# Performance work log

Hardware: AMD Instinct MI355X
Metric: run time of the kernel (lower is better)

## Reference

```python
import jax, jax.numpy as jnp
import numpy as np

B, T, F1, F2 = 16384, 5, 300, 251
IN, H = 551, 128

def setup_inputs() -> dict:
    key = jax.random.key(0)
    ks = jax.random.split(key, 16)
    s = 0.05
    return {
        "x1": jax.random.normal(ks[0], (B, T, F1), jnp.float32),
        "x2": jax.random.normal(ks[1], (B, T, F2), jnp.float32),
        "W_ih": jax.random.normal(ks[2], (4 * H, IN), jnp.float32) * s,
        "W_hh": jax.random.normal(ks[3], (4 * H, H), jnp.float32) * s,
        "b_ih": jax.random.normal(ks[4], (4 * H,), jnp.float32) * s,
        "b_hh": jax.random.normal(ks[5], (4 * H,), jnp.float32) * s,
        "W1": jax.random.normal(ks[6], (531, H * T), jnp.float32) * s,
        "b1": jax.random.normal(ks[7], (531,), jnp.float32) * s,
        "W2": jax.random.normal(ks[8], (256, 531), jnp.float32) * s,
        "b2": jax.random.normal(ks[9], (256,), jnp.float32) * s,
        "W3": jax.random.normal(ks[10], (64, 256), jnp.float32) * s,
        "b3": jax.random.normal(ks[11], (64,), jnp.float32) * s,
        "W4": jax.random.normal(ks[12], (2, 64), jnp.float32) * s,
        "b4": jax.random.normal(ks[13], (2,), jnp.float32) * s,
    }

def _lstm(x, W_ih, W_hh, b_ih, b_hh):
    # x: [B, T, IN] -> outputs [B, T, H]; PyTorch gate order i, f, g, o
    xg = jnp.einsum('bti,gi->btg', x, W_ih) + b_ih + b_hh  # [B, T, 4H]
    xg = jnp.transpose(xg, (1, 0, 2))  # [T, B, 4H]
    h0 = jnp.zeros((x.shape[0], H), x.dtype)
    c0 = jnp.zeros((x.shape[0], H), x.dtype)

    def step(carry, xg_t):
        h, c = carry
        g = xg_t + h @ W_hh.T  # [B, 4H]
        i, f, gg, o = jnp.split(g, 4, axis=-1)
        c = jax.nn.sigmoid(f) * c + jax.nn.sigmoid(i) * jnp.tanh(gg)
        h = jax.nn.sigmoid(o) * jnp.tanh(c)
        return (h, c), h

    _, hs = jax.lax.scan(step, (h0, c0), xg)  # hs: [T, B, H]
    return jnp.transpose(hs, (1, 0, 2))

def reference(x1, x2, W_ih, W_hh, b_ih, b_hh, W1, b1, W2, b2, W3, b3, W4, b4):
    x = jnp.concatenate((x1, x2), axis=2)  # [B, T, 551]
    h = _lstm(x, W_ih, W_hh, b_ih, b_hh)   # [B, T, H]
    h = h.reshape(h.shape[0], T * H)
    h = jax.nn.relu(h @ W1.T + b1)
    h = jax.nn.relu(h @ W2.T + b2)
    h = jax.nn.relu(h @ W3.T + b3)
    logits = h @ W4.T + b4
    return jax.nn.softmax(logits, axis=1)
```

## Files before the change

kernel.cpp:

```cpp
#include <hip/hip_runtime.h>
#include <hip/hip_bf16.h>


typedef short  short8  __attribute__((ext_vector_type(8)));
typedef short  short4v __attribute__((ext_vector_type(4)));
typedef float  f32x4   __attribute__((ext_vector_type(4)));

#define MFMA(a, b, c) __builtin_amdgcn_mfma_f32_16x16x32_bf16((a), (b), (c), 0, 0, 0)
#define WAITV(N) asm volatile("s_waitcnt vmcnt(" #N ")" ::: "memory")
#define LGKM0()  asm volatile("s_waitcnt lgkmcnt(0)" ::: "memory")
#define MEMF()   asm volatile("" ::: "memory")
#define BAR()    __builtin_amdgcn_s_barrier()

__device__ __forceinline__ short f2bs(float f) {
    __hip_bfloat16 h = __float2bfloat16(f);
    union { __hip_bfloat16 h; short s; } u; u.h = h; return u.s;
}
__device__ __forceinline__ float b2f(short s) {
    union { unsigned u; float f; } v; v.u = ((unsigned)(unsigned short)s) << 16; return v.f;
}
__device__ __forceinline__ float sigf(float x)  { return 1.f / (1.f + __expf(-x)); }
__device__ __forceinline__ float mytanh(float x){ return 2.f / (1.f + __expf(-2.f * x)) - 1.f; }

__device__ __forceinline__ void gload16(const void* g, void* l) {
    __builtin_amdgcn_global_load_lds(
        (const __attribute__((address_space(1))) void*)g,
        (__attribute__((address_space(3))) void*)l, 16, 0, 0);
}

#define BB     16384
#define TT     5
#define F1     300
#define F2     251
#define INF    551
#define KP     576
#define G4     512
#define HH     128
#define FLAT   640
#define L1N    531
#define L1P    576
#define L1KP   544
#define L2N    256
#define L3N    64

#define O_WIH  0u
#define O_WHH  589824u
#define O_W1   720896u
#define O_W2   1458176u
#define O_W3   1736704u
#define O_BG   1769472u
#define O_B1   1771520u
#define O_XG   1773824u
#define O_HS   85659904u
#define WS_NEED 106631424u

__device__ __forceinline__ void pack_b(const float* __restrict__ W, short* __restrict__ dst,
                                       int i, int tpn, int Nsrc, int Ksrc, int ldw)
{
    int tile = i >> 9, rem = i & 511, lane = rem >> 3, jj = rem & 7;
    int tn = tile / tpn, tk = tile - tn * tpn;
    int n = tn * 16 + (lane & 15);
    int k = tk * 32 + (lane >> 4) * 8 + jj;
    float v = (n < Nsrc && k < Ksrc) ? W[n * ldw + k] : 0.f;
    dst[i] = f2bs(v);
}

__device__ __forceinline__ void pack_bih(const float* __restrict__ W, short* __restrict__ dst,
                                         int i)
{
    int tile = i >> 9, rem = i & 511, lane = rem >> 3, jj = rem & 7;
    int tn = tile / 18, tk = tile - tn * 18;
    int n = tn * 16 + (lane & 15);
    int k = tk * 32 + (lane >> 4) * 8 + jj;
    int keff = (k <= 546) ? k : (k >= 548 && k <= 551) ? (k - 1) : -1;
    float v = (keff >= 0) ? W[n * INF + keff] : 0.f;
    dst[i] = f2bs(v);
}

__global__ void prep_kernel(
    const float* __restrict__ W_ih, const float* __restrict__ W_hh,
    const float* __restrict__ b_ih, const float* __restrict__ b_hh,
    const float* __restrict__ W1,   const float* __restrict__ b1,
    const float* __restrict__ W2,   const float* __restrict__ W3,
    short* __restrict__ Wihp, short* __restrict__ Whhp, float* __restrict__ biasg,
    short* __restrict__ W1p,  float* __restrict__ b1p,  short* __restrict__ W2p,
    short* __restrict__ W3p)
{
    const int N0 = G4 * KP;
    const int N1 = N0 + G4 * HH;
    const int N2 = N1 + L1P * FLAT;
    const int N3 = N2 + L2N * L1KP;
    const int N4 = N3 + L3N * L2N;
    const int N5 = N4 + G4;
    const int N6 = N5 + L1P;
    const int stride = gridDim.x * blockDim.x;
    for (int i = blockIdx.x * blockDim.x + threadIdx.x; i < N6; i += stride) {
        if (i < N0)      pack_bih(W_ih, Wihp, i);
        else if (i < N1) pack_b(W_hh, Whhp, i - N0,   4, G4,  HH,  HH);
        else if (i < N2) pack_b(W1,   W1p,  i - N1,  20, L1N, FLAT, FLAT);
        else if (i < N3) pack_b(W2,   W2p,  i - N2,  17, L2N, L1N, L1N);
        else if (i < N4) pack_b(W3,   W3p,  i - N3,   8, L3N, L2N, L2N);
        else if (i < N5) { int j = i - N4; biasg[j] = b_ih[j] + b_hh[j]; }
        else             { int j = i - N5; b1p[j] = (j < L1N) ? b1[j] : 0.f; }
    }
}

__device__ __forceinline__ float4 ld4r(const float* __restrict__ x1r,
                                       const float* __restrict__ x2r, int c)
{
    const float* p = (c < F1) ? (x1r + c) : (x2r + (c - F1));
    return *(const float4*)p;
}

__global__ __launch_bounds__(256, 3) void k1_xgemm(
    const float* __restrict__ x1, const float* __restrict__ x2,
    const short* __restrict__ Wihp, const float* __restrict__ biasg,
    short* __restrict__ xg)
{
    __shared__ __align__(16) short As[128][32];
    __shared__ __align__(16) short Bs[8][512];
    const int tid  = threadIdx.x;
    const int w    = tid >> 6;
    const int lane = tid & 63;
    const int c16  = lane & 15;
    const int kq   = lane >> 4;
    const int wm   = w >> 1, wn = w & 1;

    const int id  = blockIdx.x;
    const int mp  = (id & 7) * 80 + ((id >> 3) >> 2);
    const int nb  = (id >> 3) & 3;
    const int m0  = mp * 128;
    const int t   = m0 >> 14;
    const int bb  = m0 & 16383;

    const int sr = tid >> 1, sh = tid & 1;
    const int arow = bb + sr;
    const float* x1r = x1 + ((size_t)arow * TT + t) * F1;
    const float* x2r = x2 + ((size_t)arow * TT + t) * F2;
    const int fA = (sr >> 1) & 3;
    short* d0 = &As[sr][(((sh << 1)    ) ^ fA) << 3];
    short* d1 = &As[sr][(((sh << 1) | 1) ^ fA) << 3];

    f32x4 acc[4][4];
#pragma unroll
    for (int mt = 0; mt < 4; ++mt)
#pragma unroll
        for (int nt = 0; nt < 4; ++nt)
            acc[mt][nt] = (f32x4){0.f, 0.f, 0.f, 0.f};

    for (int s = 0; s < 18; ++s) {
        BAR(); MEMF();
#pragma unroll
        for (int i2 = 0; i2 < 2; ++i2) {
            int tnl = w * 2 + i2;
            gload16(Wihp + (((nb * 8 + tnl) * 18 + s) << 9) + lane * 8,
                    &Bs[tnl][0]);
        }
        float4 q0, q1, q2, q3;
        if (s < 17) {
            int c0 = s * 32 + sh * 16;
            q0 = ld4r(x1r, x2r, c0);
            q1 = ld4r(x1r, x2r, c0 + 4);
            q2 = ld4r(x1r, x2r, c0 + 8);
            q3 = ld4r(x1r, x2r, c0 + 12);
        } else {
            if (sh == 0) {
                q0 = *(const float4*)(x2r + 244);
                q1 = *(const float4*)(x2r + 247);
            } else {
                q0 = (float4){0.f, 0.f, 0.f, 0.f};
                q1 = q0;
            }
            q2 = (float4){0.f, 0.f, 0.f, 0.f};
            q3 = q2;
        }
        {
            short8 v0, v1;
            v0[0] = f2bs(q0.x); v0[1] = f2bs(q0.y); v0[2] = f2bs(q0.z); v0[3] = f2bs(q0.w);
            v0[4] = f2bs(q1.x); v0[5] = f2bs(q1.y); v0[6] = f2bs(q1.z); v0[7] = f2bs(q1.w);
            v1[0] = f2bs(q2.x); v1[1] = f2bs(q2.y); v1[2] = f2bs(q2.z); v1[3] = f2bs(q2.w);
            v1[4] = f2bs(q3.x); v1[5] = f2bs(q3.y); v1[6] = f2bs(q3.z); v1[7] = f2bs(q3.w);
            *(short8*)d0 = v0;
            *(short8*)d1 = v1;
        }
        WAITV(0); LGKM0(); BAR(); MEMF();

        short8 a[4];
#pragma unroll
        for (int mt = 0; mt < 4; ++mt) {
            int r = (wm * 4 + mt) * 16 + c16;
            a[mt] = *(const short8*)&As[r][(kq ^ ((r >> 1) & 3)) << 3];
        }
#pragma unroll
        for (int nt = 0; nt < 4; ++nt) {
            short8 b = *(const short8*)&Bs[wn * 4 + nt][lane * 8];
#pragma unroll
            for (int mt = 0; mt < 4; ++mt)
                acc[mt][nt] = MFMA(a[mt], b, acc[mt][nt]);
        }
    }

#pragma unroll
    for (int nt = 0; nt < 4; ++nt) {
        int tn = nb * 8 + wn * 4 + nt;
        float bv = biasg[tn * 16 + c16];
#pragma unroll
        for (int mt = 0; mt < 4; ++mt) {
            short4v o;
#pragma unroll
            for (int r = 0; r < 4; ++r) o[r] = f2bs(acc[mt][nt][r] + bv);
            int tm = (m0 >> 4) + wm * 4 + mt;
            *(short4v*)&xg[((tm * 32 + tn) << 8) + lane * 4] = o;
        }
    }
}

__global__ __launch_bounds__(512, 2) void k2_rec(
    const short* __restrict__ Whhp, const short* __restrict__ xg,
    short* __restrict__ hs)
{
    __shared__ __align__(16) short hb[2][32][136];
    const int tid  = threadIdx.x;
    const int w    = tid >> 6;
    const int lane = tid & 63;
    const int quad = lane >> 4;
    const int c16  = lane & 15;
    const int btile = blockIdx.x * 2;

    short8 bfr[4][4];
#pragma unroll
    for (int g = 0; g < 4; ++g)
#pragma unroll
        for (int ks = 0; ks < 4; ++ks)
            bfr[g][ks] = *(const short8*)&Whhp[((((g * 8 + w) * 4) + ks) << 9) + lane * 8];

    float cst[2][4];
#pragma unroll
    for (int mt = 0; mt < 2; ++mt)
#pragma unroll
        for (int r = 0; r < 4; ++r) cst[mt][r] = 0.f;

    const int j = w * 16 + c16;

    for (int t = 0; t < TT; ++t) {
        short4v xq[2][4];
#pragma unroll
        for (int mt = 0; mt < 2; ++mt)
#pragma unroll
            for (int g = 0; g < 4; ++g)
                xq[mt][g] = *(const short4v*)
                    &xg[((((t << 10) + btile + mt) * 32 + (g * 8 + w)) << 8) + lane * 4];

        f32x4 acc[2][4];
#pragma unroll
        for (int mt = 0; mt < 2; ++mt)
#pragma unroll
            for (int g = 0; g < 4; ++g)
                acc[mt][g] = (f32x4){0.f, 0.f, 0.f, 0.f};

        if (t > 0) {
            const short (*cur)[136] = hb[(t - 1) & 1];
#pragma unroll
            for (int ks = 0; ks < 4; ++ks) {
                short8 a[2];
#pragma unroll
                for (int mt = 0; mt < 2; ++mt)
                    a[mt] = *(const short8*)&cur[mt * 16 + c16][ks * 32 + quad * 8];
#pragma unroll
                for (int mt = 0; mt < 2; ++mt)
#pragma unroll
                    for (int g = 0; g < 4; ++g)
                        acc[mt][g] = MFMA(a[mt], bfr[g][ks], acc[mt][g]);
            }
        }

        short (*nxt)[136] = hb[t & 1];
#pragma unroll
        for (int mt = 0; mt < 2; ++mt) {
#pragma unroll
            for (int r = 0; r < 4; ++r) {
                int m = mt * 16 + quad * 4 + r;
                float gi = acc[mt][0][r] + b2f(xq[mt][0][r]);
                float gf = acc[mt][1][r] + b2f(xq[mt][1][r]);
                float gg = acc[mt][2][r] + b2f(xq[mt][2][r]);
                float go = acc[mt][3][r] + b2f(xq[mt][3][r]);
                float cn = sigf(gf) * cst[mt][r] + sigf(gi) * mytanh(gg);
                cst[mt][r] = cn;
                nxt[m][j] = f2bs(sigf(go) * mytanh(cn));
            }
        }
        __syncthreads();
        {
            int tm = w >> 2, kt = w & 3;
            short8 v = *(const short8*)&nxt[tm * 16 + c16][kt * 32 + quad * 8];
            *(short8*)&hs[(((btile + tm) * 20 + t * 4 + kt) << 9) + lane * 8] = v;
        }
    }
}

__global__ __launch_bounds__(256, 2) void mlp_kernel(
    const short* __restrict__ hs,
    const short* __restrict__ W1p, const float* __restrict__ b1p,
    const short* __restrict__ W2p, const float* __restrict__ b2,
    const short* __restrict__ W3p, const float* __restrict__ b3,
    const float* __restrict__ W4,  const float* __restrict__ b4,
    float* __restrict__ out)
{
    __shared__ __align__(16) short a1[32][584];
    __shared__ __align__(16) short a2[32][264];
    __shared__ __align__(16) short a3[32][72];
    const int tid  = threadIdx.x;
    const int w    = tid >> 6;
    const int lane = tid & 63;
    const int quad = lane >> 4;
    const int c16  = lane & 15;
    const int m0   = blockIdx.x * 32;
    const int mtile = blockIdx.x * 2;

    {
        f32x4 acc[2][9];
#pragma unroll
        for (int mt = 0; mt < 2; ++mt)
#pragma unroll
            for (int i = 0; i < 9; ++i)
                acc[mt][i] = (f32x4){0.f, 0.f, 0.f, 0.f};
#pragma unroll 4
        for (int ks = 0; ks < 20; ++ks) {
            short8 a[2];
#pragma unroll
            for (int mt = 0; mt < 2; ++mt)
                a[mt] = *(const short8*)&hs[(((mtile + mt) * 20 + ks) << 9) + lane * 8];
#pragma unroll
            for (int i = 0; i < 9; ++i) {
                short8 b = *(const short8*)&W1p[(((w * 9 + i) * 20 + ks) << 9) + lane * 8];
                acc[0][i] = MFMA(a[0], b, acc[0][i]);
                acc[1][i] = MFMA(a[1], b, acc[1][i]);
            }
        }
#pragma unroll
        for (int i = 0; i < 9; ++i) {
            int n = (w * 9 + i) * 16 + c16;
            float bv = b1p[n];
#pragma unroll
            for (int mt = 0; mt < 2; ++mt)
#pragma unroll
                for (int r = 0; r < 4; ++r) {
                    int m = mt * 16 + quad * 4 + r;
                    float v = acc[mt][i][r] + bv;
                    a1[m][n] = f2bs(v > 0.f ? v : 0.f);
                }
        }
    }
    __syncthreads();

    {
        f32x4 acc[2][4];
#pragma unroll
        for (int mt = 0; mt < 2; ++mt)
#pragma unroll
            for (int i = 0; i < 4; ++i)
                acc[mt][i] = (f32x4){0.f, 0.f, 0.f, 0.f};
#pragma unroll 4
        for (int ks = 0; ks < 17; ++ks) {
            short8 a[2];
#pragma unroll
            for (int mt = 0; mt < 2; ++mt)
                a[mt] = *(const short8*)&a1[mt * 16 + c16][ks * 32 + quad * 8];
#pragma unroll
            for (int i = 0; i < 4; ++i) {
                short8 b = *(const short8*)&W2p[(((w * 4 + i) * 17 + ks) << 9) + lane * 8];
                acc[0][i] = MFMA(a[0], b, acc[0][i]);
                acc[1][i] = MFMA(a[1], b, acc[1][i]);
            }
        }
#pragma unroll
        for (int i = 0; i < 4; ++i) {
            int n = (w * 4 + i) * 16 + c16;
            float bv = b2[n];
#pragma unroll
            for (int mt = 0; mt < 2; ++mt)
#pragma unroll
                for (int r = 0; r < 4; ++r) {
                    int m = mt * 16 + quad * 4 + r;
                    float v = acc[mt][i][r] + bv;
                    a2[m][n] = f2bs(v > 0.f ? v : 0.f);
                }
        }
    }
    __syncthreads();

    {
        f32x4 acc[2];
        acc[0] = (f32x4){0.f, 0.f, 0.f, 0.f};
        acc[1] = (f32x4){0.f, 0.f, 0.f, 0.f};
#pragma unroll
        for (int ks = 0; ks < 8; ++ks) {
            short8 a[2];
#pragma unroll
            for (int mt = 0; mt < 2; ++mt)
                a[mt] = *(const short8*)&a2[mt * 16 + c16][ks * 32 + quad * 8];
            short8 b = *(const short8*)&W3p[((w * 8 + ks) << 9) + lane * 8];
            acc[0] = MFMA(a[0], b, acc[0]);
            acc[1] = MFMA(a[1], b, acc[1]);
        }
        int n = w * 16 + c16;
        float bv = b3[n];
#pragma unroll
        for (int mt = 0; mt < 2; ++mt)
#pragma unroll
            for (int r = 0; r < 4; ++r) {
                int m = mt * 16 + quad * 4 + r;
                float v = acc[mt][r] + bv;
                a3[m][n] = f2bs(v > 0.f ? v : 0.f);
            }
    }
    __syncthreads();

    if (tid < 64) {
        int m   = tid >> 1;
        int cls = tid & 1;
        float s = b4[cls];
#pragma unroll 8
        for (int k = 0; k < 64; ++k)
            s += b2f(a3[m][k]) * W4[cls * 64 + k];
        float other = __shfl_xor(s, 1);
        float p = 1.f / (1.f + __expf(other - s));
        out[(m0 + m) * 2 + cls] = p;
    }
}

extern "C" void kernel_launch(void* const* d_in, const int* in_sizes, int n_in,
                              void* d_out, int out_size, void* d_ws, size_t ws_size,
                              hipStream_t stream)
{
    (void)in_sizes; (void)n_in; (void)out_size;
    if (ws_size < (size_t)WS_NEED) return;

    const float* x1   = (const float*)d_in[0];
    const float* x2   = (const float*)d_in[1];
    const float* W_ih = (const float*)d_in[2];
    const float* W_hh = (const float*)d_in[3];
    const float* b_ih = (const float*)d_in[4];
    const float* b_hh = (const float*)d_in[5];
    const float* W1   = (const float*)d_in[6];
    const float* b1   = (const float*)d_in[7];
    const float* W2   = (const float*)d_in[8];
    const float* b2   = (const float*)d_in[9];
    const float* W3   = (const float*)d_in[10];
    const float* b3   = (const float*)d_in[11];
    const float* W4   = (const float*)d_in[12];
    const float* b4   = (const float*)d_in[13];

    char* ws = (char*)d_ws;
    short* Wihp  = (short*)(ws + O_WIH);
    short* Whhp  = (short*)(ws + O_WHH);
    short* W1p   = (short*)(ws + O_W1);
    short* W2p   = (short*)(ws + O_W2);
    short* W3p   = (short*)(ws + O_W3);
    float* biasg = (float*)(ws + O_BG);
    float* b1p   = (float*)(ws + O_B1);
    short* xg    = (short*)(ws + O_XG);
    short* hsb   = (short*)(ws + O_HS);

    prep_kernel<<<3461, 256, 0, stream>>>(W_ih, W_hh, b_ih, b_hh, W1, b1, W2, W3,
                                          Wihp, Whhp, biasg, W1p, b1p, W2p, W3p);
    k1_xgemm<<<2560, 256, 0, stream>>>(x1, x2, Wihp, biasg, xg);
    k2_rec<<<512, 512, 0, stream>>>(Whhp, xg, hsb);
    mlp_kernel<<<512, 256, 0, stream>>>(hsb, W1p, b1p, W2p, b2, W3p, b3, W4, b4,
                                        (float*)d_out);
}
```

Before: 398.9 us.

## Double-buffer LDS tiles in input-projection GEMM to overlap loads with MFMA

The input-projection GEMM kernel now uses two LDS buffers for the A and B tiles. The next K-step's global loads and bf16 conversion are issued before the current step's MFMAs, which removes one barrier per iteration and lets load latency overlap compute. The tail-column handling moves from W_ih packing into the activation load: the packed weights use the plain layout and the last x2 float4 is shifted in-register. Doubling shared memory per block may reduce occupancy under the declared launch bounds.

```diff
diff --git a/kernel.cpp b/kernel.cpp
--- a/kernel.cpp
+++ b/kernel.cpp
@@ -65,18 +65,6 @@
     dst[i] = f2bs(v);
 }
 
-__device__ __forceinline__ void pack_bih(const float* __restrict__ W, short* __restrict__ dst,
-                                         int i)
-{
-    int tile = i >> 9, rem = i & 511, lane = rem >> 3, jj = rem & 7;
-    int tn = tile / 18, tk = tile - tn * 18;
-    int n = tn * 16 + (lane & 15);
-    int k = tk * 32 + (lane >> 4) * 8 + jj;
-    int keff = (k <= 546) ? k : (k >= 548 && k <= 551) ? (k - 1) : -1;
-    float v = (keff >= 0) ? W[n * INF + keff] : 0.f;
-    dst[i] = f2bs(v);
-}
-
 __global__ void prep_kernel(
     const float* __restrict__ W_ih, const float* __restrict__ W_hh,
     const float* __restrict__ b_ih, const float* __restrict__ b_hh,
@@ -95,7 +83,7 @@
     const int N6 = N5 + L1P;
     const int stride = gridDim.x * blockDim.x;
     for (int i = blockIdx.x * blockDim.x + threadIdx.x; i < N6; i += stride) {
-        if (i < N0)      pack_bih(W_ih, Wihp, i);
+        if (i < N0)      pack_b(W_ih, Wihp, i,       18, G4,  INF, INF);
         else if (i < N1) pack_b(W_hh, Whhp, i - N0,   4, G4,  HH,  HH);
         else if (i < N2) pack_b(W1,   W1p,  i - N1,  20, L1N, FLAT, FLAT);
         else if (i < N3) pack_b(W2,   W2p,  i - N2,  17, L2N, L1N, L1N);
@@ -117,8 +105,8 @@
     const short* __restrict__ Wihp, const float* __restrict__ biasg,
     short* __restrict__ xg)
 {
-    __shared__ __align__(16) short As[128][32];
-    __shared__ __align__(16) short Bs[8][512];
+    __shared__ __align__(16) short As[2][128][32];
+    __shared__ __align__(16) short Bs[2][8][512];
     const int tid  = threadIdx.x;
     const int w    = tid >> 6;
     const int lane = tid & 63;
@@ -137,9 +125,9 @@
     const int arow = bb + sr;
     const float* x1r = x1 + ((size_t)arow * TT + t) * F1;
     const float* x2r = x2 + ((size_t)arow * TT + t) * F2;
-    const int fA = (sr >> 1) & 3;
-    short* d0 = &As[sr][(((sh << 1)    ) ^ fA) << 3];
-    short* d1 = &As[sr][(((sh << 1) | 1) ^ fA) << 3];
+    const int fA  = (sr >> 1) & 3;
+    const int ch0 = ((sh << 1)    ) ^ fA;
+    const int ch1 = ((sh << 1) | 1) ^ fA;
 
     f32x4 acc[4][4];
 #pragma unroll
@@ -148,17 +136,40 @@
         for (int nt = 0; nt < 4; ++nt)
             acc[mt][nt] = (f32x4){0.f, 0.f, 0.f, 0.f};
 
-    for (int s = 0; s < 18; ++s) {
-        BAR(); MEMF();
+    {
 #pragma unroll
         for (int i2 = 0; i2 < 2; ++i2) {
             int tnl = w * 2 + i2;
-            gload16(Wihp + (((nb * 8 + tnl) * 18 + s) << 9) + lane * 8,
-                    &Bs[tnl][0]);
+            gload16(Wihp + (((nb * 8 + tnl) * 18 + 0) << 9) + lane * 8,
+                    &Bs[0][tnl][0]);
+        }
+        int c0 = sh * 16;
+        float4 q0 = ld4r(x1r, x2r, c0);
+        float4 q1 = ld4r(x1r, x2r, c0 + 4);
+        float4 q2 = ld4r(x1r, x2r, c0 + 8);
+        float4 q3 = ld4r(x1r, x2r, c0 + 12);
+        short8 v0, v1;
+        v0[0]=f2bs(q0.x); v0[1]=f2bs(q0.y); v0[2]=f2bs(q0.z); v0[3]=f2bs(q0.w);
+        v0[4]=f2bs(q1.x); v0[5]=f2bs(q1.y); v0[6]=f2bs(q1.z); v0[7]=f2bs(q1.w);
+        v1[0]=f2bs(q2.x); v1[1]=f2bs(q2.y); v1[2]=f2bs(q2.z); v1[3]=f2bs(q2.w);
+        v1[4]=f2bs(q3.x); v1[5]=f2bs(q3.y); v1[6]=f2bs(q3.z); v1[7]=f2bs(q3.w);
+        *(short8*)&As[0][sr][ch0 << 3] = v0;
+        *(short8*)&As[0][sr][ch1 << 3] = v1;
+    }
+    WAITV(0); LGKM0(); BAR(); MEMF();
+
+    for (int s = 0; s < 17; ++s) {
+        const int nbuf = (s + 1) & 1, cbuf = s & 1;
+
+#pragma unroll
+        for (int i2 = 0; i2 < 2; ++i2) {
+            int tnl = w * 2 + i2;
+            gload16(Wihp + (((nb * 8 + tnl) * 18 + (s + 1)) << 9) + lane * 8,
+                    &Bs[nbuf][tnl][0]);
         }
         float4 q0, q1, q2, q3;
-        if (s < 17) {
-            int c0 = s * 32 + sh * 16;
+        if (s + 1 < 17) {
+            int c0 = (s + 1) * 32 + sh * 16;
             q0 = ld4r(x1r, x2r, c0);
             q1 = ld4r(x1r, x2r, c0 + 4);
             q2 = ld4r(x1r, x2r, c0 + 8);
@@ -166,7 +177,8 @@
         } else {
             if (sh == 0) {
                 q0 = *(const float4*)(x2r + 244);
-                q1 = *(const float4*)(x2r + 247);
+                float4 qt = *(const float4*)(x2r + 247);
+                q1 = (float4){qt.y, qt.z, qt.w, 0.f};
             } else {
                 q0 = (float4){0.f, 0.f, 0.f, 0.f};
                 q1 = q0;
@@ -174,26 +186,45 @@
             q2 = (float4){0.f, 0.f, 0.f, 0.f};
             q3 = q2;
         }
+
+        {
+            short8 a[4];
+#pragma unroll
+            for (int mt = 0; mt < 4; ++mt) {
+                int r = (wm * 4 + mt) * 16 + c16;
+                a[mt] = *(const short8*)&As[cbuf][r][(kq ^ ((r >> 1) & 3)) << 3];
+            }
+#pragma unroll
+            for (int nt = 0; nt < 4; ++nt) {
+                short8 b = *(const short8*)&Bs[cbuf][wn * 4 + nt][lane * 8];
+#pragma unroll
+                for (int mt = 0; mt < 4; ++mt)
+                    acc[mt][nt] = MFMA(a[mt], b, acc[mt][nt]);
+            }
+        }
+
         {
             short8 v0, v1;
-            v0[0] = f2bs(q0.x); v0[1] = f2bs(q0.y); v0[2] = f2bs(q0.z); v0[3] = f2bs(q0.w);
-            v0[4] = f2bs(q1.x); v0[5] = f2bs(q1.y); v0[6] = f2bs(q1.z); v0[7] = f2bs(q1.w);
-            v1[0] = f2bs(q2.x); v1[1] = f2bs(q2.y); v1[2] = f2bs(q2.z); v1[3] = f2bs(q2.w);
-            v1[4] = f2bs(q3.x); v1[5] = f2bs(q3.y); v1[6] = f2bs(q3.z); v1[7] = f2bs(q3.w);
-            *(short8*)d0 = v0;
-            *(short8*)d1 = v1;
+            v0[0]=f2bs(q0.x); v0[1]=f2bs(q0.y); v0[2]=f2bs(q0.z); v0[3]=f2bs(q0.w);
+            v0[4]=f2bs(q1.x); v0[5]=f2bs(q1.y); v0[6]=f2bs(q1.z); v0[7]=f2bs(q1.w);
+            v1[0]=f2bs(q2.x); v1[1]=f2bs(q2.y); v1[2]=f2bs(q2.z); v1[3]=f2bs(q2.w);
+            v1[4]=f2bs(q3.x); v1[5]=f2bs(q3.y); v1[6]=f2bs(q3.z); v1[7]=f2bs(q3.w);
+            *(short8*)&As[nbuf][sr][ch0 << 3] = v0;
+            *(short8*)&As[nbuf][sr][ch1 << 3] = v1;
         }
         WAITV(0); LGKM0(); BAR(); MEMF();
-
+    }
+
+    {
         short8 a[4];
 #pragma unroll
         for (int mt = 0; mt < 4; ++mt) {
             int r = (wm * 4 + mt) * 16 + c16;
-            a[mt] = *(const short8*)&As[r][(kq ^ ((r >> 1) & 3)) << 3];
+            a[mt] = *(const short8*)&As[1][r][(kq ^ ((r >> 1) & 3)) << 3];
         }
 #pragma unroll
         for (int nt = 0; nt < 4; ++nt) {
-            short8 b = *(const short8*)&Bs[wn * 4 + nt][lane * 8];
+            short8 b = *(const short8*)&Bs[1][wn * 4 + nt][lane * 8];
 #pragma unroll
             for (int mt = 0; mt < 4; ++mt)
                 acc[mt][nt] = MFMA(a[mt], b, acc[mt][nt]);
```

Result: slower. 435.6 us (+9.2%).
